# Optimization experiments

Hardware: AMD Instinct MI355X
Metric: run time of the kernel (lower is better)

## Reference

```python
import jax, jax.numpy as jnp
import numpy as np

D = 2  # spatial dimension


def _conv_contract(image, filt, in_k, out_k):
    """Tensor convolution + contraction on a torus.
    image: (in_c, N, N) + (D,)*in_k
    filt:  (out_c, in_c, M, M) + (D,)*in_k + (D,)*out_k
    out:   (out_c, N, N) + (D,)*out_k
    Image tensor indices contract with the first in_k filter tensor indices.
    """
    in_c, N = image.shape[0], image.shape[1]
    out_c, M = filt.shape[0], filt.shape[2]
    di, do = D ** in_k, D ** out_k
    # fold tensor indices into channels: (1, in_c*di, N, N)
    img = jnp.transpose(image.reshape(in_c, N, N, di), (0, 3, 1, 2)).reshape(1, in_c * di, N, N)
    # filter -> (out_c*do, in_c*di, M, M), ordering (out_c, out_idx, in_c, in_idx)
    f = filt.reshape(out_c, in_c, M, M, di, do)
    f = jnp.transpose(f, (0, 5, 1, 4, 2, 3)).reshape(out_c * do, in_c * di, M, M)
    p = M // 2
    img = jnp.pad(img, ((0, 0), (0, 0), (p, p), (p, p)), mode='wrap')  # torus
    out = jax.lax.conv_general_dilated(
        img, f, window_strides=(1, 1), padding='VALID',
        dimension_numbers=('NCHW', 'OIHW', 'NCHW'))[0]
    out = jnp.transpose(out.reshape(out_c, do, N, N), (0, 2, 3, 1))
    return out.reshape((out_c, N, N) + (D,) * out_k)


def _synth(w, fils):
    # (out_c, in_c, n) x (n, M, M, tensor...) -> (out_c, in_c, M, M, tensor...)
    return jnp.einsum('oik,k...->oi...', w, fils)


def setup_inputs() -> dict:
    key = jax.random.key(0)
    ks = jax.random.split(key, 11)
    r = lambda k, s: jax.random.normal(k, s, dtype=jnp.float32)
    return {
        'x0': r(ks[0], (64, 256, 256)),
        'x1': r(ks[1], (64, 256, 256, 2)),
        'fil0': r(ks[2], (3, 3, 3)),
        'fil1': r(ks[3], (6, 3, 3, 2)),
        'fil2': r(ks[4], (12, 3, 3, 2, 2)),
        'w00': r(ks[5], (64, 64, 3)) * (1.0 / np.sqrt(64 * 3)),
        'w01': r(ks[6], (64, 64, 6)) * (1.0 / np.sqrt(64 * 6)),
        'w10': r(ks[7], (64, 64, 6)) * (1.0 / np.sqrt(64 * 6)),
        'w11': r(ks[8], (64, 64, 12)) * (1.0 / np.sqrt(64 * 12)),
        'b0': r(ks[9], (64, 1, 1)) * 0.05,
        'b1': r(ks[10], (64, 1, 1, 1)) * 0.05,
    }


def reference(x0, x1, fil0, fil1, fil2, w00, w01, w10, w11, b0, b1):
    # accumulate over input blocks for each target (out_k, out_p=0)
    out0 = _conv_contract(x0, _synth(w00, fil0), 0, 0) \
         + _conv_contract(x1, _synth(w10, fil1), 1, 0)
    out1 = _conv_contract(x0, _synth(w01, fil1), 0, 1) \
         + _conv_contract(x1, _synth(w11, fil2), 1, 1)
    # use_bias='auto': plain bias for scalars, mean-scaled bias for tensors
    out0 = out0 + b0
    mean1 = jnp.mean(out1, axis=(1, 2), keepdims=True)  # spatial mean
    out1 = out1 + mean1 * b1
    return (out0, out1)
```

## Files before the change

kernel.cpp:

```cpp
#include <hip/hip_runtime.h>
#include <hip/hip_bf16.h>
#include <string.h>


#define NN 256
#define NPIX 65536
#define OUT1_OFF 4194304
#define FS 192
#define FBYT 36864
#define XBYT 24576
#define BUFB 61440

typedef __attribute__((ext_vector_type(8))) short short8;
typedef __attribute__((ext_vector_type(4))) float floatx4;

__device__ __forceinline__ unsigned short f2b(float x) {
    unsigned int u; memcpy(&u, &x, 4);
    return (unsigned short)((u + 0x7FFFu + ((u >> 16) & 1u)) >> 16);
}
__device__ __forceinline__ float b2f16(unsigned short u) {
    unsigned int v = ((unsigned int)u) << 16; float f; memcpy(&f, &v, 4); return f;
}
__device__ __forceinline__ unsigned int pack2(float a, float b) {
    return (unsigned int)f2b(a) | ((unsigned int)f2b(b) << 16);
}

__global__ __launch_bounds__(256) void prep_kernel(const float* __restrict__ x0,
                                                   const float* __restrict__ x1,
                                                   unsigned short* __restrict__ Xb,
                                                   float* __restrict__ partial) {
    const int t = threadIdx.x;
    const int w = t >> 6, tx = t & 63;
    const int y = blockIdx.x * 4 + w;
    const int c = blockIdx.y;
    const int col0 = tx * 4;

    unsigned int u[4][8];
    float sum[16];
    if (c < 4) {
        #pragma unroll
        for (int j = 0; j < 8; j++) {
            const float4 a = *(const float4*)(x0 + (size_t)(16 * c + 2 * j) * NPIX + y * NN + col0);
            const float4 b = *(const float4*)(x0 + (size_t)(16 * c + 2 * j + 1) * NPIX + y * NN + col0);
            u[0][j] = pack2(a.x, b.x);
            u[1][j] = pack2(a.y, b.y);
            u[2][j] = pack2(a.z, b.z);
            u[3][j] = pack2(a.w, b.w);
            sum[2 * j]     = a.x + a.y + a.z + a.w;
            sum[2 * j + 1] = b.x + b.y + b.z + b.w;
        }
    } else {
        #pragma unroll
        for (int j = 0; j < 8; j++) {
            int i = 8 * (c - 4) + j;
            const float* base = x1 + ((size_t)(i * 256 + y) * 256 + col0) * 2;
            const float4 p0 = *(const float4*)(base);
            const float4 p1 = *(const float4*)(base + 4);
            u[0][j] = pack2(p0.x, p0.y);
            u[1][j] = pack2(p0.z, p0.w);
            u[2][j] = pack2(p1.x, p1.y);
            u[3][j] = pack2(p1.z, p1.w);
            sum[2 * j]     = p0.x + p0.z + p1.x + p1.z;
            sum[2 * j + 1] = p0.y + p0.w + p1.y + p1.w;
        }
    }
    char* rowp = (char*)(Xb + ((size_t)y * 12 + c) * 4096);
    #pragma unroll
    for (int cc = 0; cc < 4; cc++) {
        int col = col0 + cc;
        int sw = ((col >> 3) & 7) << 4;
        *(uint4*)(rowp + ((col * 32)      ^ sw)) = make_uint4(u[cc][0], u[cc][1], u[cc][2], u[cc][3]);
        *(uint4*)(rowp + ((col * 32 + 16) ^ sw)) = make_uint4(u[cc][4], u[cc][5], u[cc][6], u[cc][7]);
    }
    #pragma unroll
    for (int cl = 0; cl < 16; cl++)
        #pragma unroll
        for (int d = 1; d < 64; d <<= 1) sum[cl] += __shfl_xor(sum[cl], d, 64);
    if (tx < 16) partial[(c * 16 + tx) * 256 + y] = sum[tx];
}

__global__ void synth_kernel(const float* __restrict__ fil0, const float* __restrict__ fil1,
                             const float* __restrict__ fil2,
                             const float* __restrict__ w00, const float* __restrict__ w01,
                             const float* __restrict__ w10, const float* __restrict__ w11,
                             unsigned short* __restrict__ Fb) {
    int idx = blockIdx.x * 256 + threadIdx.x;
    if (idx >= 12 * 192 * FS) return;
    int kpos = idx % FS;
    int co   = (idx / FS) % 192;
    int c    = idx / (FS * 192);
    int tap = kpos >> 4, cl = kpos & 15;
    float s = 0.0f;
    if (tap < 9) {
        int cin = c * 16 + cl;
        if (co < 64) {
            if (cin < 64) {
                for (int k = 0; k < 3; k++)
                    s += w00[(co * 64 + cin) * 3 + k] * fil0[k * 9 + tap];
            } else {
                int i = (cin - 64) >> 1, t = (cin - 64) & 1;
                for (int k = 0; k < 6; k++)
                    s += w10[(co * 64 + i) * 6 + k] * fil1[(k * 9 + tap) * 2 + t];
            }
        } else {
            int o = (co - 64) >> 1, u = (co - 64) & 1;
            if (cin < 64) {
                for (int k = 0; k < 6; k++)
                    s += w01[(o * 64 + cin) * 6 + k] * fil1[(k * 9 + tap) * 2 + u];
            } else {
                int i = (cin - 64) >> 1, t = (cin - 64) & 1;
                for (int k = 0; k < 12; k++)
                    s += w11[(o * 64 + i) * 12 + k] * fil2[((k * 9 + tap) * 2 + t) * 2 + u];
            }
        }
    }
    Fb[((size_t)c * 192 + co) * FS + (kpos ^ ((co & 7) << 3))] = f2b(s);
}

__global__ void meanbx_kernel(const unsigned short* __restrict__ Fb,
                              const float* __restrict__ partial,
                              const float* __restrict__ b1, float* __restrict__ meanb) {
    __shared__ float mX[192];
    __shared__ float rd[4];
    const int c1 = blockIdx.x;
    const int t = threadIdx.x;
    if (t < 192) {
        const float4* p = (const float4*)(partial + (size_t)t * 256);
        float s = 0.0f;
        for (int j = 0; j < 64; j++) { float4 v = p[j]; s += v.x + v.y + v.z + v.w; }
        mX[t] = s * (1.0f / 65536.0f);
    }
    __syncthreads();
    float s = 0.0f;
    for (int e = t; e < 1728; e += 256) {
        int c = e / 144, r = e - c * 144;
        int tap = r >> 4, cl = r & 15;
        s += b2f16(Fb[((size_t)c * 192 + 64 + c1) * FS + ((tap * 16 + cl) ^ ((c1 & 7) << 3))])
             * mX[c * 16 + cl];
    }
#pragma unroll
    for (int d = 1; d < 64; d <<= 1) s += __shfl_xor(s, d, 64);
    if ((t & 63) == 0) rd[t >> 6] = s;
    __syncthreads();
    if (t == 0) meanb[c1] = (rd[0] + rd[1] + rd[2] + rd[3]) * b1[c1 >> 1];
}

__global__ __launch_bounds__(512, 2) void conv_kernel(
    const unsigned short* __restrict__ Xb, const unsigned short* __restrict__ Fb,
    const float* __restrict__ b0, const float* __restrict__ meanb,
    float* __restrict__ out) {

    __shared__ __align__(16) char lds[2 * BUFB];

    const int tid = threadIdx.x;
    const int y = blockIdx.x;
    const int m0 = blockIdx.y * 96;
    const int l = tid & 63, w = tid >> 6;
    const int wm = w >> 2, wn = w & 3;
    const int mw = wm * 48, nw = wn * 64;
    const int ln = l & 15, quad = l >> 4;

    int addrA[5][3];
    int addrB[5][4];
    const int swzA = (ln & 7) << 4;
#pragma unroll
    for (int ks = 0; ks < 5; ks++) {
#pragma unroll
        for (int f = 0; f < 3; f++) {
            int row = mw + f * 16 + ln;
            addrA[ks][f] = (row * (FS * 2) + quad * 16 + ks * 64) ^ swzA;
        }
        int tap = 2 * ks + (quad >> 1);
        int r, dx;
        if (tap > 8) { r = 0; dx = 0; }
        else { r = tap / 3; dx = tap - 3 * r - 1; }
#pragma unroll
        for (int g = 0; g < 4; g++) {
            int colw = (nw + g * 16 + ln + dx) & 255;
            addrB[ks][g] = FBYT + r * 8192 +
                ((colw * 32 + (quad & 1) * 16) ^ (((colw >> 3) & 7) << 4));
        }
    }

    floatx4 acc[3][4];
#pragma unroll
    for (int f = 0; f < 3; f++)
#pragma unroll
        for (int g = 0; g < 4; g++) acc[f][g] = (floatx4){0.f, 0.f, 0.f, 0.f};

    auto stage = [&](int c, int bsel) {
        const unsigned short* FbC = Fb + ((size_t)c * 192 + m0) * FS;
        char* base = lds + bsel * BUFB;
        for (int s = w; s < 60; s += 8) {
            const unsigned short* g;
            char* lb;
            if (s < 36) {
                g = FbC + s * 512;
                lb = base + s * 1024;
            } else {
                int j = s - 36;
                int r = j >> 3, p = j & 7;
                int yr = (y + r + 255) & 255;
                g = Xb + ((size_t)yr * 12 + c) * 4096 + p * 512;
                lb = base + FBYT + r * 8192 + p * 1024;
            }
            __builtin_amdgcn_global_load_lds(
                (const __attribute__((address_space(1))) unsigned int*)(g + l * 8),
                (__attribute__((address_space(3))) unsigned int*)lb, 16, 0, 0);
        }
    };

    stage(0, 0);
    __syncthreads();

    int cur = 0;
    for (int c = 0; c < 12; c++) {
        if (c < 11) stage(c + 1, cur ^ 1);
        const char* fb = lds + cur * BUFB;
#pragma unroll
        for (int ks = 0; ks < 5; ks++) {
            short8 A[3], B[4];
#pragma unroll
            for (int f = 0; f < 3; f++) A[f] = *(const short8*)(fb + addrA[ks][f]);
#pragma unroll
            for (int g = 0; g < 4; g++) B[g] = *(const short8*)(fb + addrB[ks][g]);
#pragma unroll
            for (int f = 0; f < 3; f++)
#pragma unroll
                for (int g = 0; g < 4; g++)
                    acc[f][g] = __builtin_amdgcn_mfma_f32_16x16x32_bf16(A[f], B[g], acc[f][g], 0, 0, 0);
        }
        __syncthreads();
        cur ^= 1;
    }

#pragma unroll
    for (int f = 0; f < 3; f++) {
        int cob = m0 + mw + f * 16 + quad * 4;
#pragma unroll
        for (int g = 0; g < 4; g++) {
            int col = nw + g * 16 + ln;
            if (cob < 64) {
#pragma unroll
                for (int reg = 0; reg < 4; reg++)
                    out[(size_t)(cob + reg) * NPIX + y * NN + col] = acc[f][g][reg] + b0[cob + reg];
            } else {
#pragma unroll
                for (int reg = 0; reg < 4; reg += 2) {
                    int c1 = cob + reg - 64;
                    int o = c1 >> 1;
                    float2 v = make_float2(acc[f][g][reg] + meanb[c1],
                                           acc[f][g][reg + 1] + meanb[c1 + 1]);
                    *((float2*)(out + OUT1_OFF) + ((size_t)o * NPIX + y * NN + col)) = v;
                }
            }
        }
    }
}

extern "C" void kernel_launch(void* const* d_in, const int* in_sizes, int n_in,
                              void* d_out, int out_size, void* d_ws, size_t ws_size,
                              hipStream_t stream) {
    const float* x0   = (const float*)d_in[0];
    const float* x1   = (const float*)d_in[1];
    const float* fil0 = (const float*)d_in[2];
    const float* fil1 = (const float*)d_in[3];
    const float* fil2 = (const float*)d_in[4];
    const float* w00  = (const float*)d_in[5];
    const float* w01  = (const float*)d_in[6];
    const float* w10  = (const float*)d_in[7];
    const float* w11  = (const float*)d_in[8];
    const float* b0   = (const float*)d_in[9];
    const float* b1   = (const float*)d_in[10];

    unsigned short* Xb = (unsigned short*)d_ws;
    unsigned short* Fb = (unsigned short*)((char*)d_ws + 25165824);
    float* partial     = (float*)((char*)d_ws + 26050560);
    float* meanb       = (float*)((char*)d_ws + 26247168);
    float* out = (float*)d_out;

    prep_kernel<<<dim3(64, 12), 256, 0, stream>>>(x0, x1, Xb, partial);

    synth_kernel<<<(12 * 192 * FS + 255) / 256, 256, 0, stream>>>(
        fil0, fil1, fil2, w00, w01, w10, w11, Fb);

    meanbx_kernel<<<128, 256, 0, stream>>>(Fb, partial, b1, meanb);

    conv_kernel<<<dim3(NN, 2), 512, 0, stream>>>(Xb, Fb, b0, meanb, out);
}
```

Measured before the change: 187.0 us.

## Load filter fragments directly from global in MFMA layout, shrink LDS to image tiles

The filter weights are now synthesized directly into a per-lane MFMA fragment layout, so the conv kernel reads the A operands straight from global memory and cache instead of staging them in LDS. LDS holds only the three image rows per channel chunk, which cuts the per-block footprint and lets launch bounds ask for 4 blocks per CU. Block-to-row mapping is also permuted in both the prep and conv kernels, which changes which rows run concurrently and so may affect cache locality. The cost is global or cache latency on the A loads inside the MFMA loop, with no double buffering for them.

```diff
diff --git a/kernel.cpp b/kernel.cpp
--- a/kernel.cpp
+++ b/kernel.cpp
@@ -6,10 +6,9 @@
 #define NN 256
 #define NPIX 65536
 #define OUT1_OFF 4194304
-#define FS 192
-#define FBYT 36864
-#define XBYT 24576
-#define BUFB 61440
+#define XB_CH 4096
+#define FG_C 30720
+#define XTILE 24576
 
 typedef __attribute__((ext_vector_type(8))) short short8;
 typedef __attribute__((ext_vector_type(4))) float floatx4;
@@ -31,7 +30,9 @@
                                                    float* __restrict__ partial) {
     const int t = threadIdx.x;
     const int w = t >> 6, tx = t & 63;
-    const int y = blockIdx.x * 4 + w;
+    const int bxs = blockIdx.x;
+    const int yg = ((bxs & 7) << 3) | (bxs >> 3);
+    const int y = yg * 4 + w;
     const int c = blockIdx.y;
     const int col0 = tx * 4;
 
@@ -64,7 +65,7 @@
             sum[2 * j + 1] = p0.y + p0.w + p1.y + p1.w;
         }
     }
-    char* rowp = (char*)(Xb + ((size_t)y * 12 + c) * 4096);
+    char* rowp = (char*)(Xb + ((size_t)y * 12 + c) * XB_CH);
     #pragma unroll
     for (int cc = 0; cc < 4; cc++) {
         int col = col0 + cc;
@@ -83,12 +84,19 @@
                              const float* __restrict__ fil2,
                              const float* __restrict__ w00, const float* __restrict__ w01,
                              const float* __restrict__ w10, const float* __restrict__ w11,
-                             unsigned short* __restrict__ Fb) {
+                             unsigned short* __restrict__ Fg) {
     int idx = blockIdx.x * 256 + threadIdx.x;
-    if (idx >= 12 * 192 * FS) return;
-    int kpos = idx % FS;
-    int co   = (idx / FS) % 192;
-    int c    = idx / (FS * 192);
+    if (idx >= 12 * 12 * 5 * 512) return;
+    int sub = idx & 511;
+    int blk = idx >> 9;
+    int ks = blk % 5;
+    int rc = blk / 5;
+    int rt = rc % 12;
+    int c = rc / 12;
+    int lane = sub >> 3, j = sub & 7;
+    int quad = lane >> 4, ln = lane & 15;
+    int co = rt * 16 + ln;
+    int kpos = ks * 32 + quad * 8 + j;
     int tap = kpos >> 4, cl = kpos & 15;
     float s = 0.0f;
     if (tap < 9) {
@@ -114,10 +122,10 @@
             }
         }
     }
-    Fb[((size_t)c * 192 + co) * FS + (kpos ^ ((co & 7) << 3))] = f2b(s);
-}
-
-__global__ void meanbx_kernel(const unsigned short* __restrict__ Fb,
+    Fg[idx] = f2b(s);
+}
+
+__global__ void meanbx_kernel(const unsigned short* __restrict__ Fg,
                               const float* __restrict__ partial,
                               const float* __restrict__ b1, float* __restrict__ meanb) {
     __shared__ float mX[192];
@@ -134,9 +142,10 @@
     float s = 0.0f;
     for (int e = t; e < 1728; e += 256) {
         int c = e / 144, r = e - c * 144;
-        int tap = r >> 4, cl = r & 15;
-        s += b2f16(Fb[((size_t)c * 192 + 64 + c1) * FS + ((tap * 16 + cl) ^ ((c1 & 7) << 3))])
-             * mX[c * 16 + cl];
+        int cl = r & 15;
+        int fidx = ((c * 12 + 4 + (c1 >> 4)) * 5 + (r >> 5)) * 512
+                 + ((((r >> 3) & 3) * 16 + (c1 & 15)) << 3) + (r & 7);
+        s += b2f16(Fg[fidx]) * mX[c * 16 + cl];
     }
 #pragma unroll
     for (int d = 1; d < 64; d <<= 1) s += __shfl_xor(s, d, 64);
@@ -145,31 +154,32 @@
     if (t == 0) meanb[c1] = (rd[0] + rd[1] + rd[2] + rd[3]) * b1[c1 >> 1];
 }
 
-__global__ __launch_bounds__(512, 2) void conv_kernel(
-    const unsigned short* __restrict__ Xb, const unsigned short* __restrict__ Fb,
+__global__ __launch_bounds__(512, 4) void conv_kernel(
+    const unsigned short* __restrict__ Xb, const unsigned short* __restrict__ Fg,
     const float* __restrict__ b0, const float* __restrict__ meanb,
     float* __restrict__ out) {
 
-    __shared__ __align__(16) char lds[2 * BUFB];
+    __shared__ __align__(16) char lds[2 * XTILE];
 
     const int tid = threadIdx.x;
-    const int y = blockIdx.x;
+    const int bx = blockIdx.x;
+    const int y = ((bx & 7) << 5) | (bx >> 3);
     const int m0 = blockIdx.y * 96;
     const int l = tid & 63, w = tid >> 6;
     const int wm = w >> 2, wn = w & 3;
-    const int mw = wm * 48, nw = wn * 64;
+    const int nw = wn * 64;
     const int ln = l & 15, quad = l >> 4;
 
-    int addrA[5][3];
+    const unsigned short* pF[3];
+#pragma unroll
+    for (int f = 0; f < 3; f++) {
+        int rt = blockIdx.y * 6 + wm * 3 + f;
+        pF[f] = Fg + ((size_t)rt * 320 + l) * 8;
+    }
+
     int addrB[5][4];
-    const int swzA = (ln & 7) << 4;
 #pragma unroll
     for (int ks = 0; ks < 5; ks++) {
-#pragma unroll
-        for (int f = 0; f < 3; f++) {
-            int row = mw + f * 16 + ln;
-            addrA[ks][f] = (row * (FS * 2) + quad * 16 + ks * 64) ^ swzA;
-        }
         int tap = 2 * ks + (quad >> 1);
         int r, dx;
         if (tap > 8) { r = 0; dx = 0; }
@@ -177,7 +187,7 @@
 #pragma unroll
         for (int g = 0; g < 4; g++) {
             int colw = (nw + g * 16 + ln + dx) & 255;
-            addrB[ks][g] = FBYT + r * 8192 +
+            addrB[ks][g] = r * 8192 +
                 ((colw * 32 + (quad & 1) * 16) ^ (((colw >> 3) & 7) << 4));
         }
     }
@@ -189,24 +199,15 @@
         for (int g = 0; g < 4; g++) acc[f][g] = (floatx4){0.f, 0.f, 0.f, 0.f};
 
     auto stage = [&](int c, int bsel) {
-        const unsigned short* FbC = Fb + ((size_t)c * 192 + m0) * FS;
-        char* base = lds + bsel * BUFB;
-        for (int s = w; s < 60; s += 8) {
-            const unsigned short* g;
-            char* lb;
-            if (s < 36) {
-                g = FbC + s * 512;
-                lb = base + s * 1024;
-            } else {
-                int j = s - 36;
-                int r = j >> 3, p = j & 7;
-                int yr = (y + r + 255) & 255;
-                g = Xb + ((size_t)yr * 12 + c) * 4096 + p * 512;
-                lb = base + FBYT + r * 8192 + p * 1024;
-            }
+        char* base = lds + bsel * XTILE;
+#pragma unroll
+        for (int i = 0; i < 3; i++) {
+            int yr = (y + i + 255) & 255;
+            const unsigned short* g = Xb + ((size_t)yr * 12 + c) * XB_CH + w * 512;
             __builtin_amdgcn_global_load_lds(
                 (const __attribute__((address_space(1))) unsigned int*)(g + l * 8),
-                (__attribute__((address_space(3))) unsigned int*)lb, 16, 0, 0);
+                (__attribute__((address_space(3))) unsigned int*)(base + i * 8192 + w * 1024),
+                16, 0, 0);
         }
     };
 
@@ -214,26 +215,31 @@
     __syncthreads();
 
     int cur = 0;
+    size_t coff = 0;
     for (int c = 0; c < 12; c++) {
         if (c < 11) stage(c + 1, cur ^ 1);
-        const char* fb = lds + cur * BUFB;
+        const char* xb = lds + cur * XTILE;
 #pragma unroll
         for (int ks = 0; ks < 5; ks++) {
             short8 A[3], B[4];
 #pragma unroll
-            for (int f = 0; f < 3; f++) A[f] = *(const short8*)(fb + addrA[ks][f]);
-#pragma unroll
-            for (int g = 0; g < 4; g++) B[g] = *(const short8*)(fb + addrB[ks][g]);
+            for (int f = 0; f < 3; f++)
+                A[f] = *(const short8*)(pF[f] + coff + ks * 512);
+#pragma unroll
+            for (int g = 0; g < 4; g++)
+                B[g] = *(const short8*)(xb + addrB[ks][g]);
 #pragma unroll
             for (int f = 0; f < 3; f++)
 #pragma unroll
                 for (int g = 0; g < 4; g++)
                     acc[f][g] = __builtin_amdgcn_mfma_f32_16x16x32_bf16(A[f], B[g], acc[f][g], 0, 0, 0);
         }
+        coff += FG_C;
         __syncthreads();
         cur ^= 1;
     }
 
+    const int mw = wm * 48;
 #pragma unroll
     for (int f = 0; f < 3; f++) {
         int cob = m0 + mw + f * 16 + quad * 4;
@@ -274,17 +280,17 @@
     const float* b1   = (const float*)d_in[10];
 
     unsigned short* Xb = (unsigned short*)d_ws;
-    unsigned short* Fb = (unsigned short*)((char*)d_ws + 25165824);
-    float* partial     = (float*)((char*)d_ws + 26050560);
-    float* meanb       = (float*)((char*)d_ws + 26247168);
+    unsigned short* Fg = (unsigned short*)((char*)d_ws + 25165824);
+    float* partial     = (float*)((char*)d_ws + 25903104);
+    float* meanb       = (float*)((char*)d_ws + 26099712);
     float* out = (float*)d_out;
 
     prep_kernel<<<dim3(64, 12), 256, 0, stream>>>(x0, x1, Xb, partial);
 
-    synth_kernel<<<(12 * 192 * FS + 255) / 256, 256, 0, stream>>>(
-        fil0, fil1, fil2, w00, w01, w10, w11, Fb);
-
-    meanbx_kernel<<<128, 256, 0, stream>>>(Fb, partial, b1, meanb);
-
-    conv_kernel<<<dim3(NN, 2), 512, 0, stream>>>(Xb, Fb, b0, meanb, out);
-}
+    synth_kernel<<<(12 * 12 * 5 * 512 + 255) / 256, 256, 0, stream>>>(
+        fil0, fil1, fil2, w00, w01, w10, w11, Fg);
+
+    meanbx_kernel<<<128, 256, 0, stream>>>(Fg, partial, b1, meanb);
+
+    conv_kernel<<<dim3(NN, 2), 512, 0, stream>>>(Xb, Fg, b0, meanb, out);
+}
```

Result: no change. 184.1 us (-1.5%).
